# Performance work log

Hardware: AMD Instinct MI355X
Metric: run time of the kernel (lower is better)

## Reference

```python
import jax, jax.numpy as jnp
import numpy as np

LN_EPS = 1e-5
OPM_EPS = 1e-3


def setup_inputs() -> dict:
    key = jax.random.key(0)
    ks = jax.random.split(key, 8)
    S, N, c_m, c_h, c_z = 128, 256, 256, 32, 128
    m = jax.random.normal(ks[0], (S, N, c_m), dtype=jnp.float32)
    mask = jnp.ones((S, N), dtype=jnp.float32)
    ln_w = jnp.ones((c_m,), dtype=jnp.float32)
    ln_b = jnp.zeros((c_m,), dtype=jnp.float32)
    sc1 = 1.0 / np.sqrt(c_m)
    w1 = jax.random.uniform(ks[1], (c_m, c_h), jnp.float32, -sc1, sc1)
    b1 = jax.random.uniform(ks[2], (c_h,), jnp.float32, -sc1, sc1)
    w2 = jax.random.uniform(ks[3], (c_m, c_h), jnp.float32, -sc1, sc1)
    b2 = jax.random.uniform(ks[4], (c_h,), jnp.float32, -sc1, sc1)
    sco = 1.0 / np.sqrt(c_h * c_h)
    wo = jax.random.uniform(ks[5], (c_h * c_h, c_z), jnp.float32, -sco, sco)
    bo = jax.random.uniform(ks[6], (c_z,), jnp.float32, -sco, sco)
    return {"m": m, "mask": mask, "ln_w": ln_w, "ln_b": ln_b,
            "w1": w1, "b1": b1, "w2": w2, "b2": b2, "wo": wo, "bo": bo}


def reference(m, mask, ln_w, ln_b, w1, b1, w2, b2, wo, bo):
    # LayerNorm over c_m
    mu = jnp.mean(m, axis=-1, keepdims=True)
    var = jnp.var(m, axis=-1, keepdims=True)
    ln = (m - mu) * jax.lax.rsqrt(var + LN_EPS) * ln_w + ln_b
    mk = mask[..., None]                       # [S, N, 1]
    a = (ln @ w1 + b1) * mk                    # [S, N, c_h]
    b = (ln @ w2 + b2) * mk                    # [S, N, c_h]
    # outer-product mean over the MSA dim s: [N, N, c_h, c_h]
    S, N, ch = a.shape
    outer = jnp.einsum('sic,sjd->ijcd', a, b).reshape(N, N, ch * ch)
    outer = outer @ wo + bo                    # [N, N, c_z]
    norm = jnp.einsum('si,sj->ij', mask, mask)[..., None] + OPM_EPS
    return outer / norm
```

## Files before the change

kernel.cpp:

```cpp
#include <hip/hip_runtime.h>
#include <hip/hip_bf16.h>

typedef __attribute__((ext_vector_type(8))) short short8;
typedef __attribute__((ext_vector_type(4))) short short4v;
typedef __attribute__((ext_vector_type(4))) float float4v;

#define S_DIM 128
#define N_DIM 256
#define CM    256
#define CH    32
#define CZ    128

#define AS1 __attribute__((address_space(1)))
#define AS3 __attribute__((address_space(3)))

static __device__ __forceinline__ short f2bf(float v) {
    return __builtin_bit_cast(short, __float2bfloat16(v));
}


__global__ __launch_bounds__(256) void prep_aux_kernel(
    const float* __restrict__ m, const float* __restrict__ mask,
    const float* __restrict__ lnw, const float* __restrict__ lnb,
    const float* __restrict__ w1, const float* __restrict__ b1,
    const float* __restrict__ w2, const float* __restrict__ b2,
    const float* __restrict__ wo, const float* __restrict__ bo,
    __hip_bfloat16* __restrict__ a_f, __hip_bfloat16* __restrict__ b_f,
    __hip_bfloat16* __restrict__ wo_f, float* __restrict__ ninv)
{
    __shared__ __align__(16) char lds_raw[77824];
    __hip_bfloat16* ln_lds = (__hip_bfloat16*)lds_raw;
    __hip_bfloat16* w_lds  = (__hip_bfloat16*)(lds_raw + 33792);
    __hip_bfloat16* st_lds = (__hip_bfloat16*)(lds_raw + 67584);

    const int bid = blockIdx.x, t = threadIdx.x;

    if (bid >= 576) {
        int i0 = (bid - 576) * 4, j = t;
        float a0 = 0.f, a1 = 0.f, a2 = 0.f, a3 = 0.f;
        for (int s = 0; s < S_DIM; ++s) {
            float mj = mask[s * N_DIM + j];
            a0 += mask[s * N_DIM + i0 + 0] * mj;
            a1 += mask[s * N_DIM + i0 + 1] * mj;
            a2 += mask[s * N_DIM + i0 + 2] * mj;
            a3 += mask[s * N_DIM + i0 + 3] * mj;
        }
        ninv[(i0 + 0) * N_DIM + j] = 1.0f / (a0 + 1e-3f);
        ninv[(i0 + 1) * N_DIM + j] = 1.0f / (a1 + 1e-3f);
        ninv[(i0 + 2) * N_DIM + j] = 1.0f / (a2 + 1e-3f);
        ninv[(i0 + 3) * N_DIM + j] = 1.0f / (a3 + 1e-3f);
        return;
    }
    if (bid >= 512) {
        int fidx = (bid - 512) * 256 + t;
        int l  = fidx & 63;
        int d  = (fidx >> 6) & 31;
        int zt = fidx >> 11;
        int z  = zt * 16 + (l & 15);
        int cb = (l >> 4) * 8;
        short8 frag;
        #pragma unroll
        for (int j = 0; j < 8; ++j)
            frag[j] = f2bf(wo[(size_t)((cb + j) * 32 + d) * CZ + z]);
        *(short8*)&wo_f[(size_t)fidx * 8] = frag;
        return;
    }

    const int lane = t & 63, wv = t >> 6;
    const int q = lane >> 4, c16 = lane & 15;
    const int n0 = (bid & 127) * 2, s0 = (bid >> 7) * 32, sk = bid >> 7;

    #pragma unroll 4
    for (int i = 0; i < 64; ++i) {
        int e = i * 256 + t;
        int k = e >> 6, c = e & 63;
        float v = (c < CH) ? w1[k * CH + c] : w2[k * CH + (c - CH)];
        w_lds[c * 264 + k] = __float2bfloat16(v);
    }

    float4 lw = ((const float4*)lnw)[lane];
    float4 lb = ((const float4*)lnb)[lane];

    #pragma unroll 2
    for (int it = 0; it < 16; ++it) {
        int rl = wv * 16 + it;
        int r  = (s0 + (rl >> 1)) * N_DIM + n0 + (rl & 1);
        float4 mv = ((const float4*)(m + (size_t)r * CM))[lane];
        float s1 = mv.x + mv.y + mv.z + mv.w;
        float s2 = mv.x*mv.x + mv.y*mv.y + mv.z*mv.z + mv.w*mv.w;
        #pragma unroll
        for (int o = 32; o > 0; o >>= 1) {
            s1 += __shfl_xor(s1, o, 64);
            s2 += __shfl_xor(s2, o, 64);
        }
        float mu  = s1 * (1.0f / 256.0f);
        float var = s2 * (1.0f / 256.0f) - mu * mu;
        float rs  = rsqrtf(var + 1e-5f);
        int base = rl * 264 + lane * 4;
        ln_lds[base + 0] = __float2bfloat16((mv.x - mu) * rs * lw.x + lb.x);
        ln_lds[base + 1] = __float2bfloat16((mv.y - mu) * rs * lw.y + lb.y);
        ln_lds[base + 2] = __float2bfloat16((mv.z - mu) * rs * lw.z + lb.z);
        ln_lds[base + 3] = __float2bfloat16((mv.w - mu) * rs * lw.w + lb.w);
    }
    __syncthreads();

    float4v acc[4];
    #pragma unroll
    for (int ct = 0; ct < 4; ++ct) acc[ct] = (float4v){0.f, 0.f, 0.f, 0.f};
    #pragma unroll
    for (int ks = 0; ks < 8; ++ks) {
        int k0 = ks * 32 + q * 8;
        short8 af = *(const short8*)&ln_lds[(wv * 16 + c16) * 264 + k0];
        #pragma unroll
        for (int ct = 0; ct < 4; ++ct) {
            short8 wb = *(const short8*)&w_lds[(ct * 16 + c16) * 264 + k0];
            acc[ct] = __builtin_amdgcn_mfma_f32_16x16x32_bf16(af, wb, acc[ct], 0, 0, 0);
        }
    }

    #pragma unroll
    for (int ct = 0; ct < 4; ++ct) {
        int cc = ct * 16 + c16;
        float bias = (cc < CH) ? b1[cc] : b2[cc - CH];
        #pragma unroll
        for (int rr = 0; rr < 4; ++rr) {
            int rl = wv * 16 + q * 4 + rr;
            int r  = (s0 + (rl >> 1)) * N_DIM + n0 + (rl & 1);
            float val = (acc[ct][rr] + bias) * mask[r];
            st_lds[((rl & 1) * 64 + cc) * 40 + (rl >> 1)] = __float2bfloat16(val);
        }
    }
    __syncthreads();

    #pragma unroll
    for (int i = 0; i < 2; ++i) {
        int slot = i * 256 + t;
        int f8 = slot >> 6, l = slot & 63;
        int fl = f8 & 3, nl = fl >> 1, cch = fl & 1;
        int lq = l >> 4, lc16 = l & 15;
        int col = nl * 64 + (f8 >= 4 ? 32 : 0) + cch * 16 + lc16;
        short8 v = *(const short8*)&st_lds[col * 40 + lq * 8];
        __hip_bfloat16* base = (f8 >= 4) ? b_f : a_f;
        *(short8*)&base[(size_t)((n0 * 2 + fl) * 4 + sk) * 512 + l * 8] = v;
    }
}

__global__ __launch_bounds__(512, 4) void main_kernel(
    const __hip_bfloat16* __restrict__ a_f, const __hip_bfloat16* __restrict__ b_f,
    const __hip_bfloat16* __restrict__ wo_f, const float* __restrict__ bo,
    const float* __restrict__ ninv, float* __restrict__ out)
{
    __shared__ __align__(16) short lds[33280];

    const int t = threadIdx.x, l = t & 63, wv = t >> 6;
    const int q = l >> 4, c16 = l & 15;
    const int bi = blockIdx.x, bj0 = blockIdx.y * 2;
    const int wr = wv & 3, wc = wv >> 2;
    const size_t Ix = (size_t)bi * 8;

    #pragma unroll
    for (int tau = 0; tau < 2; ++tau) {
        const size_t Jx = (size_t)(bj0 + tau) * 8;
        #pragma unroll
        for (int i = 0; i < 4; ++i) {
            int f = i * 8 + wv;
            __builtin_amdgcn_global_load_lds(
                (AS1 const void*)&b_f[((Jx + (f >> 2)) * 4 + (f & 3)) * 512 + l * 8],
                (AS3 void*)&lds[tau * 16640 + f * 512], 16, 0, 0);
        }
    }

    short8 af[4][2];
    #pragma unroll
    for (int sk = 0; sk < 4; ++sk)
        #pragma unroll
        for (int ti = 0; ti < 2; ++ti)
            af[sk][ti] = *(const short8*)&a_f[((Ix + wr * 2 + ti) * 4 + sk) * 512 + l * 8];

    __syncthreads();

    float4v accA[2][4];
    #pragma unroll
    for (int ti = 0; ti < 2; ++ti)
        #pragma unroll
        for (int tj = 0; tj < 4; ++tj)
            accA[ti][tj] = (float4v){0.f, 0.f, 0.f, 0.f};
    #pragma unroll
    for (int sk = 0; sk < 4; ++sk) {
        short8 bf[4];
        #pragma unroll
        for (int tj = 0; tj < 4; ++tj)
            bf[tj] = *(const short8*)&lds[((wc * 4 + tj) * 4 + sk) * 512 + l * 8];
        #pragma unroll
        for (int tj = 0; tj < 4; ++tj) {
            accA[0][tj] = __builtin_amdgcn_mfma_f32_16x16x32_bf16(af[sk][0], bf[tj], accA[0][tj], 0, 0, 0);
            accA[1][tj] = __builtin_amdgcn_mfma_f32_16x16x32_bf16(af[sk][1], bf[tj], accA[1][tj], 0, 0, 0);
        }
    }
    __syncthreads();

    #pragma unroll
    for (int ti = 0; ti < 2; ++ti)
        #pragma unroll
        for (int tj = 0; tj < 4; ++tj) {
            int d  = ((tj & 1) * 16) + c16;
            int c0 = ti * 16 + q * 4;
            int p  = wr * 4 + wc * 2 + (tj >> 1);
            short4v pk;
            #pragma unroll
            for (int rr = 0; rr < 4; ++rr)
                pk[rr] = f2bf(accA[ti][tj][rr]);
            *(short4v*)&lds[d * 520 + (c0 >> 3) * 128 + p * 8 + (c0 & 7)] = pk;
        }

    float4v accB[2][4];
    #pragma unroll
    for (int ti = 0; ti < 2; ++ti)
        #pragma unroll
        for (int tj = 0; tj < 4; ++tj)
            accB[ti][tj] = (float4v){0.f, 0.f, 0.f, 0.f};
    #pragma unroll
    for (int sk = 0; sk < 4; ++sk) {
        short8 bf[4];
        #pragma unroll
        for (int tj = 0; tj < 4; ++tj)
            bf[tj] = *(const short8*)&lds[16640 + ((wc * 4 + tj) * 4 + sk) * 512 + l * 8];
        #pragma unroll
        for (int tj = 0; tj < 4; ++tj) {
            accB[0][tj] = __builtin_amdgcn_mfma_f32_16x16x32_bf16(af[sk][0], bf[tj], accB[0][tj], 0, 0, 0);
            accB[1][tj] = __builtin_amdgcn_mfma_f32_16x16x32_bf16(af[sk][1], bf[tj], accB[1][tj], 0, 0, 0);
        }
    }
    __syncthreads();

    #pragma unroll
    for (int ti = 0; ti < 2; ++ti)
        #pragma unroll
        for (int tj = 0; tj < 4; ++tj) {
            int d  = ((tj & 1) * 16) + c16;
            int c0 = ti * 16 + q * 4;
            int p  = wr * 4 + wc * 2 + (tj >> 1);
            short4v pk;
            #pragma unroll
            for (int rr = 0; rr < 4; ++rr)
                pk[rr] = f2bf(accB[ti][tj][rr]);
            *(short4v*)&lds[16640 + d * 520 + (c0 >> 3) * 128 + p * 8 + (c0 & 7)] = pk;
        }
    __syncthreads();

    float4v oacc[2];
    oacc[0] = (float4v){0.f, 0.f, 0.f, 0.f};
    oacc[1] = (float4v){0.f, 0.f, 0.f, 0.f};
    const __hip_bfloat16* wbase = wo_f + (size_t)wv * 32 * 512;
    #pragma unroll 4
    for (int d = 0; d < 32; ++d) {
        short8 p0 = *(const short8*)&lds[        d * 520 + l * 8];
        short8 p1 = *(const short8*)&lds[16640 + d * 520 + l * 8];
        short8 wf = *(const short8*)&wbase[(size_t)(d * 512 + l * 8)];
        oacc[0] = __builtin_amdgcn_mfma_f32_16x16x32_bf16(p0, wf, oacc[0], 0, 0, 0);
        oacc[1] = __builtin_amdgcn_mfma_f32_16x16x32_bf16(p1, wf, oacc[1], 0, 0, 0);
    }

    const int gi = bi * 4 + q;
    const int z  = wv * 16 + c16;
    const float bz = bo[z];
    #pragma unroll
    for (int tau = 0; tau < 2; ++tau) {
        const int bj = bj0 + tau;
        #pragma unroll
        for (int rr = 0; rr < 4; ++rr) {
            int gj = bj * 4 + rr;
            float nv = ninv[gi * N_DIM + gj];
            out[((size_t)gi * N_DIM + gj) * CZ + z] = (oacc[tau][rr] + bz) * nv;
        }
    }
}

extern "C" void kernel_launch(void* const* d_in, const int* in_sizes, int n_in,
                              void* d_out, int out_size, void* d_ws, size_t ws_size,
                              hipStream_t stream) {
    const float* m    = (const float*)d_in[0];
    const float* mask = (const float*)d_in[1];
    const float* lnw  = (const float*)d_in[2];
    const float* lnb  = (const float*)d_in[3];
    const float* w1   = (const float*)d_in[4];
    const float* b1   = (const float*)d_in[5];
    const float* w2   = (const float*)d_in[6];
    const float* b2   = (const float*)d_in[7];
    const float* wo   = (const float*)d_in[8];
    const float* bo   = (const float*)d_in[9];
    float* out = (float*)d_out;

    char* ws = (char*)d_ws;
    __hip_bfloat16* a_f  = (__hip_bfloat16*)ws;
    __hip_bfloat16* b_f  = (__hip_bfloat16*)(ws + (2u << 20));
    __hip_bfloat16* wo_f = (__hip_bfloat16*)(ws + (4u << 20));
    float*          ninv = (float*)(ws + (4u << 20) + (256u << 10));

    prep_aux_kernel<<<640, 256, 0, stream>>>(m, mask, lnw, lnb, w1, b1, w2, b2,
                                             wo, bo, a_f, b_f, wo_f, ninv);
    main_kernel<<<dim3(64, 32), 512, 0, stream>>>(a_f, b_f, wo_f, bo, ninv, out);
}
```

Baseline: 147.7 us.

## Re-tile outer-product and projection stages across waves with split-K reduction

Each wave now computes a 4x4 tile of outer-product MFMAs for one of the two j-blocks, instead of a 2x4 tile for both j-blocks in sequence. This removes one store/sync phase and loads the A fragments per k-step inside a non-unrolled loop. The output projection is split over the d dimension (K-split) across wave halves, each wave computing 2x2 z/tau tiles. The halves are combined through an LDS reduction, which raises per-wave reuse of the weight loads but adds an extra reduction pass and register pressure from 16 accumulators.

Result: faster. 144.5 us (-2.2%).

```diff
diff --git a/kernel.cpp b/kernel.cpp
--- a/kernel.cpp
+++ b/kernel.cpp
@@ -155,7 +155,6 @@
     const int t = threadIdx.x, l = t & 63, wv = t >> 6;
     const int q = l >> 4, c16 = l & 15;
     const int bi = blockIdx.x, bj0 = blockIdx.y * 2;
-    const int wr = wv & 3, wc = wv >> 2;
     const size_t Ix = (size_t)bi * 8;
 
     #pragma unroll
@@ -170,109 +169,98 @@
         }
     }
 
-    short8 af[4][2];
-    #pragma unroll
-    for (int sk = 0; sk < 4; ++sk)
-        #pragma unroll
-        for (int ti = 0; ti < 2; ++ti)
-            af[sk][ti] = *(const short8*)&a_f[((Ix + wr * 2 + ti) * 4 + sk) * 512 + l * 8];
-
-    __syncthreads();
-
-    float4v accA[2][4];
-    #pragma unroll
-    for (int ti = 0; ti < 2; ++ti)
-        #pragma unroll
-        for (int tj = 0; tj < 4; ++tj)
-            accA[ti][tj] = (float4v){0.f, 0.f, 0.f, 0.f};
-    #pragma unroll
+    const int tauW = wv & 1, Ig = (wv >> 1) & 1, Jg = wv >> 2;
+    const int RB = tauW * 16640;
+
+    float4v acc[4][4];
+    #pragma unroll
+    for (int ii = 0; ii < 4; ++ii)
+        #pragma unroll
+        for (int jj = 0; jj < 4; ++jj)
+            acc[ii][jj] = (float4v){0.f, 0.f, 0.f, 0.f};
+
+    __syncthreads();
+
+    #pragma unroll 1
     for (int sk = 0; sk < 4; ++sk) {
-        short8 bf[4];
-        #pragma unroll
-        for (int tj = 0; tj < 4; ++tj)
-            bf[tj] = *(const short8*)&lds[((wc * 4 + tj) * 4 + sk) * 512 + l * 8];
-        #pragma unroll
-        for (int tj = 0; tj < 4; ++tj) {
-            accA[0][tj] = __builtin_amdgcn_mfma_f32_16x16x32_bf16(af[sk][0], bf[tj], accA[0][tj], 0, 0, 0);
-            accA[1][tj] = __builtin_amdgcn_mfma_f32_16x16x32_bf16(af[sk][1], bf[tj], accA[1][tj], 0, 0, 0);
-        }
-    }
-    __syncthreads();
-
-    #pragma unroll
-    for (int ti = 0; ti < 2; ++ti)
-        #pragma unroll
-        for (int tj = 0; tj < 4; ++tj) {
-            int d  = ((tj & 1) * 16) + c16;
-            int c0 = ti * 16 + q * 4;
-            int p  = wr * 4 + wc * 2 + (tj >> 1);
+        short8 afr[4], bfr[4];
+        #pragma unroll
+        for (int ii = 0; ii < 4; ++ii)
+            afr[ii] = *(const short8*)&a_f[((Ix + Ig * 4 + ii) * 4 + sk) * 512 + l * 8];
+        #pragma unroll
+        for (int jj = 0; jj < 4; ++jj)
+            bfr[jj] = *(const short8*)&lds[RB + ((Jg * 4 + jj) * 4 + sk) * 512 + l * 8];
+        #pragma unroll
+        for (int jj = 0; jj < 4; ++jj)
+            #pragma unroll
+            for (int ii = 0; ii < 4; ++ii)
+                acc[ii][jj] = __builtin_amdgcn_mfma_f32_16x16x32_bf16(afr[ii], bfr[jj], acc[ii][jj], 0, 0, 0);
+    }
+    __syncthreads();
+
+    #pragma unroll
+    for (int ii = 0; ii < 4; ++ii) {
+        const int c0 = (ii & 1) * 16 + q * 4;
+        #pragma unroll
+        for (int jj = 0; jj < 4; ++jj) {
+            const int d = (jj & 1) * 16 + c16;
+            const int p = (Ig * 2 + (ii >> 1)) * 4 + Jg * 2 + (jj >> 1);
             short4v pk;
             #pragma unroll
-            for (int rr = 0; rr < 4; ++rr)
-                pk[rr] = f2bf(accA[ti][tj][rr]);
-            *(short4v*)&lds[d * 520 + (c0 >> 3) * 128 + p * 8 + (c0 & 7)] = pk;
-        }
-
-    float4v accB[2][4];
-    #pragma unroll
-    for (int ti = 0; ti < 2; ++ti)
-        #pragma unroll
-        for (int tj = 0; tj < 4; ++tj)
-            accB[ti][tj] = (float4v){0.f, 0.f, 0.f, 0.f};
-    #pragma unroll
-    for (int sk = 0; sk < 4; ++sk) {
-        short8 bf[4];
-        #pragma unroll
-        for (int tj = 0; tj < 4; ++tj)
-            bf[tj] = *(const short8*)&lds[16640 + ((wc * 4 + tj) * 4 + sk) * 512 + l * 8];
-        #pragma unroll
-        for (int tj = 0; tj < 4; ++tj) {
-            accB[0][tj] = __builtin_amdgcn_mfma_f32_16x16x32_bf16(af[sk][0], bf[tj], accB[0][tj], 0, 0, 0);
-            accB[1][tj] = __builtin_amdgcn_mfma_f32_16x16x32_bf16(af[sk][1], bf[tj], accB[1][tj], 0, 0, 0);
-        }
-    }
-    __syncthreads();
-
-    #pragma unroll
-    for (int ti = 0; ti < 2; ++ti)
-        #pragma unroll
-        for (int tj = 0; tj < 4; ++tj) {
-            int d  = ((tj & 1) * 16) + c16;
-            int c0 = ti * 16 + q * 4;
-            int p  = wr * 4 + wc * 2 + (tj >> 1);
-            short4v pk;
-            #pragma unroll
-            for (int rr = 0; rr < 4; ++rr)
-                pk[rr] = f2bf(accB[ti][tj][rr]);
-            *(short4v*)&lds[16640 + d * 520 + (c0 >> 3) * 128 + p * 8 + (c0 & 7)] = pk;
-        }
-    __syncthreads();
-
-    float4v oacc[2];
-    oacc[0] = (float4v){0.f, 0.f, 0.f, 0.f};
-    oacc[1] = (float4v){0.f, 0.f, 0.f, 0.f};
-    const __hip_bfloat16* wbase = wo_f + (size_t)wv * 32 * 512;
-    #pragma unroll 4
-    for (int d = 0; d < 32; ++d) {
-        short8 p0 = *(const short8*)&lds[        d * 520 + l * 8];
+            for (int rr = 0; rr < 4; ++rr) pk[rr] = f2bf(acc[ii][jj][rr]);
+            *(short4v*)&lds[RB + d * 520 + (c0 >> 3) * 128 + p * 8 + (c0 & 7)] = pk;
+        }
+    }
+    __syncthreads();
+
+    const int zt = wv & 3, kh = wv >> 2;
+    float4v oa00 = (float4v){0.f, 0.f, 0.f, 0.f};
+    float4v oa01 = oa00, oa10 = oa00, oa11 = oa00;
+    #pragma unroll 2
+    for (int d16 = 0; d16 < 16; ++d16) {
+        const int d = kh * 16 + d16;
+        short8 p0 = *(const short8*)&lds[d * 520 + l * 8];
         short8 p1 = *(const short8*)&lds[16640 + d * 520 + l * 8];
-        short8 wf = *(const short8*)&wbase[(size_t)(d * 512 + l * 8)];
-        oacc[0] = __builtin_amdgcn_mfma_f32_16x16x32_bf16(p0, wf, oacc[0], 0, 0, 0);
-        oacc[1] = __builtin_amdgcn_mfma_f32_16x16x32_bf16(p1, wf, oacc[1], 0, 0, 0);
+        short8 w0 = *(const short8*)&wo_f[(size_t)(zt * 64 + d) * 512 + l * 8];
+        short8 w1 = *(const short8*)&wo_f[(size_t)(zt * 64 + 32 + d) * 512 + l * 8];
+        oa00 = __builtin_amdgcn_mfma_f32_16x16x32_bf16(p0, w0, oa00, 0, 0, 0);
+        oa01 = __builtin_amdgcn_mfma_f32_16x16x32_bf16(p0, w1, oa01, 0, 0, 0);
+        oa10 = __builtin_amdgcn_mfma_f32_16x16x32_bf16(p1, w0, oa10, 0, 0, 0);
+        oa11 = __builtin_amdgcn_mfma_f32_16x16x32_bf16(p1, w1, oa11, 0, 0, 0);
+    }
+    __syncthreads();
+
+    float* red = (float*)lds;
+    const int slot = (zt * 64 + l) * 4;
+    if (kh) {
+        *(float4v*)&red[slot]        = oa00;
+        *(float4v*)&red[1024 + slot] = oa01;
+    } else {
+        *(float4v*)&red[2048 + slot] = oa10;
+        *(float4v*)&red[3072 + slot] = oa11;
+    }
+    __syncthreads();
+
+    float4v f0, f1;
+    if (kh == 0) {
+        f0 = oa00 + *(const float4v*)&red[slot];
+        f1 = oa01 + *(const float4v*)&red[1024 + slot];
+    } else {
+        f0 = oa10 + *(const float4v*)&red[2048 + slot];
+        f1 = oa11 + *(const float4v*)&red[3072 + slot];
     }
 
     const int gi = bi * 4 + q;
-    const int z  = wv * 16 + c16;
-    const float bz = bo[z];
-    #pragma unroll
-    for (int tau = 0; tau < 2; ++tau) {
-        const int bj = bj0 + tau;
-        #pragma unroll
-        for (int rr = 0; rr < 4; ++rr) {
-            int gj = bj * 4 + rr;
-            float nv = ninv[gi * N_DIM + gj];
-            out[((size_t)gi * N_DIM + gj) * CZ + z] = (oacc[tau][rr] + bz) * nv;
-        }
+    const int bj = bj0 + kh;
+    const int z0 = zt * 32 + c16;
+    const float bz0 = bo[z0], bz1 = bo[z0 + 16];
+    #pragma unroll
+    for (int rr = 0; rr < 4; ++rr) {
+        const int gj = bj * 4 + rr;
+        const float nv = ninv[gi * N_DIM + gj];
+        float* o = &out[((size_t)gi * N_DIM + gj) * CZ + z0];
+        o[0]  = (f0[rr] + bz0) * nv;
+        o[16] = (f1[rr] + bz1) * nv;
     }
 }
 
```

## Split projection K across wave pairs with 2x2 register tiles and LDS reduction

Applied to the files above, without the earlier changes.

Restructures the final projection GEMM so each wave computes a 2x2 tile (two pair-blocks by two z-tiles) over half of the d dimension, instead of one z-tile over all 32 d. Each loaded wo fragment and LDS operand is now reused twice, halving global weight traffic per MFMA and raising MFMA density per load. The two half-K partial sums are combined through an LDS reduction, which costs two extra barriers and some LDS traffic.

Result: no change. 147.6 us (-0.1%).

```diff
diff --git a/kernel.cpp b/kernel.cpp
--- a/kernel.cpp
+++ b/kernel.cpp
@@ -248,31 +248,55 @@
         }
     __syncthreads();
 
-    float4v oacc[2];
-    oacc[0] = (float4v){0.f, 0.f, 0.f, 0.f};
-    oacc[1] = (float4v){0.f, 0.f, 0.f, 0.f};
-    const __hip_bfloat16* wbase = wo_f + (size_t)wv * 32 * 512;
+    const int zt = wv & 3, kh = wv >> 2;
+    float4v oa00 = (float4v){0.f, 0.f, 0.f, 0.f};
+    float4v oa01 = oa00, oa10 = oa00, oa11 = oa00;
+    const __hip_bfloat16* wb0 = wo_f + ((size_t)((zt * 2 + 0) * 32 + kh * 16)) * 512;
+    const __hip_bfloat16* wb1 = wo_f + ((size_t)((zt * 2 + 1) * 32 + kh * 16)) * 512;
+    const short* pb = &lds[kh * 16 * 520 + l * 8];
     #pragma unroll 4
-    for (int d = 0; d < 32; ++d) {
-        short8 p0 = *(const short8*)&lds[        d * 520 + l * 8];
-        short8 p1 = *(const short8*)&lds[16640 + d * 520 + l * 8];
-        short8 wf = *(const short8*)&wbase[(size_t)(d * 512 + l * 8)];
-        oacc[0] = __builtin_amdgcn_mfma_f32_16x16x32_bf16(p0, wf, oacc[0], 0, 0, 0);
-        oacc[1] = __builtin_amdgcn_mfma_f32_16x16x32_bf16(p1, wf, oacc[1], 0, 0, 0);
+    for (int d16 = 0; d16 < 16; ++d16) {
+        short8 p0 = *(const short8*)&pb[d16 * 520];
+        short8 p1 = *(const short8*)&pb[16640 + d16 * 520];
+        short8 w0 = *(const short8*)&wb0[(size_t)d16 * 512 + l * 8];
+        short8 w1 = *(const short8*)&wb1[(size_t)d16 * 512 + l * 8];
+        oa00 = __builtin_amdgcn_mfma_f32_16x16x32_bf16(p0, w0, oa00, 0, 0, 0);
+        oa01 = __builtin_amdgcn_mfma_f32_16x16x32_bf16(p0, w1, oa01, 0, 0, 0);
+        oa10 = __builtin_amdgcn_mfma_f32_16x16x32_bf16(p1, w0, oa10, 0, 0, 0);
+        oa11 = __builtin_amdgcn_mfma_f32_16x16x32_bf16(p1, w1, oa11, 0, 0, 0);
+    }
+    __syncthreads();
+
+    float* red = (float*)lds;
+    if (kh) {
+        *(float4v*)&red[(((zt * 2 + 0) * 2 + 1) * 64 + l) * 4] = oa00;
+        *(float4v*)&red[(((zt * 2 + 1) * 2 + 1) * 64 + l) * 4] = oa01;
+    } else {
+        *(float4v*)&red[(((zt * 2 + 0) * 2 + 0) * 64 + l) * 4] = oa10;
+        *(float4v*)&red[(((zt * 2 + 1) * 2 + 0) * 64 + l) * 4] = oa11;
+    }
+    __syncthreads();
+
+    float4v f0, f1;
+    if (kh == 0) {
+        f0 = oa00 + *(const float4v*)&red[(((zt * 2 + 0) * 2 + 1) * 64 + l) * 4];
+        f1 = oa01 + *(const float4v*)&red[(((zt * 2 + 1) * 2 + 1) * 64 + l) * 4];
+    } else {
+        f0 = oa10 + *(const float4v*)&red[(((zt * 2 + 0) * 2 + 0) * 64 + l) * 4];
+        f1 = oa11 + *(const float4v*)&red[(((zt * 2 + 1) * 2 + 0) * 64 + l) * 4];
     }
 
     const int gi = bi * 4 + q;
-    const int z  = wv * 16 + c16;
-    const float bz = bo[z];
-    #pragma unroll
-    for (int tau = 0; tau < 2; ++tau) {
-        const int bj = bj0 + tau;
-        #pragma unroll
-        for (int rr = 0; rr < 4; ++rr) {
-            int gj = bj * 4 + rr;
-            float nv = ninv[gi * N_DIM + gj];
-            out[((size_t)gi * N_DIM + gj) * CZ + z] = (oacc[tau][rr] + bz) * nv;
-        }
+    const int bj = bj0 + kh;
+    const int z0 = zt * 32 + c16;
+    const float bz0 = bo[z0], bz1 = bo[z0 + 16];
+    #pragma unroll
+    for (int rr = 0; rr < 4; ++rr) {
+        int gj = bj * 4 + rr;
+        float nv = ninv[gi * N_DIM + gj];
+        float* o = &out[((size_t)gi * N_DIM + gj) * CZ + z0];
+        o[0]  = (f0[rr] + bz0) * nv;
+        o[16] = (f1[rr] + bz1) * nv;
     }
 }
 
```
